# Performance work log

Measured on AMD Instinct MI355X. Metric: run time of the kernel, lower is better.

## Reference

```python
import jax, jax.numpy as jnp
import numpy as np

B, H, N, D = 2, 12, 2048, 64
M = int(D * np.log(D))          # 266 performer random features
E3 = 3 * D                      # performer value hidden size = head_dim*3
DH2 = 2 * D                     # predictor enc hidden = head_dim*2
T = 128                         # attention_predictor_length
CHUNK = 128                     # chunk size for causal linear attention scan
KERNEL_EPS = 1e-3               # performer generalized-kernel epsilon
D_EPS = 1e-6                    # denominator epsilon (added to k_cumsum)
LN_EPS = 1e-5


def setup_inputs() -> dict:
    key = jax.random.key(0)
    ks = jax.random.split(key, 10)
    return {
        "q": jax.random.normal(ks[0], (B, H, N, D), jnp.float32),
        "k": jax.random.normal(ks[1], (B, H, N, D), jnp.float32),
        "v3": jax.random.normal(ks[2], (B, H, N, E3), jnp.float32),
        "proj": jax.random.normal(ks[3], (M, D), jnp.float32),
        "enc_w": jax.random.normal(ks[4], (E3, DH2), jnp.float32) * 0.05,
        "enc_b": jnp.zeros((DH2,), jnp.float32),
        "ln_g": jnp.ones((DH2,), jnp.float32),
        "ln_b": jnp.zeros((DH2,), jnp.float32),
        "dec_w": jax.random.normal(ks[5], (DH2, T), jnp.float32) * 0.05,
        "dec_b": jnp.zeros((T,), jnp.float32),
    }


def _generalized_features(x, proj):
    # performer generalized attention kernel: relu((x / d^0.25) @ proj^T) + eps
    dn = 1.0 / (x.shape[-1] ** 0.25)
    xp = jnp.einsum("bhnd,md->bhnm", x * dn, proj)
    return jax.nn.relu(xp) + KERNEL_EPS


def _causal_linear_attention(qf, kf, v):
    # qf, kf: [B,H,N,M]; v: [B,H,N,E]. Chunked recurrent form of
    # out[n] = (qf[n] . cumsum(kf)[n])^-1 * qf[n] @ cumsum(kf[m] v[m]^T)[n]
    nE = v.shape[-1]
    nc = N // CHUNK
    qc = qf.reshape(B, H, nc, CHUNK, M).transpose(2, 0, 1, 3, 4)
    kc = kf.reshape(B, H, nc, CHUNK, M).transpose(2, 0, 1, 3, 4)
    vc = v.reshape(B, H, nc, CHUNK, nE).transpose(2, 0, 1, 3, 4)
    mask = jnp.tril(jnp.ones((CHUNK, CHUNK), qf.dtype))

    def step(carry, inp):
        ksum, S = carry                      # [B,H,M], [B,H,M,E]
        q_c, k_c, v_c = inp                  # [B,H,C,M], [B,H,C,M], [B,H,C,E]
        qk = jnp.einsum("bhim,bhjm->bhij", q_c, k_c) * mask  # causal within chunk
        # denominator: qf[n] . (k_cumsum[n] + eps)
        d = (jnp.einsum("bhcm,bhm->bhc", q_c, ksum)
             + qk.sum(-1)
             + D_EPS * q_c.sum(-1))
        out = (jnp.einsum("bhcm,bhme->bhce", q_c, S)
               + jnp.einsum("bhij,bhje->bhie", qk, v_c)) / d[..., None]
        ksum = ksum + k_c.sum(axis=2)
        S = S + jnp.einsum("bhcm,bhce->bhme", k_c, v_c)
        return (ksum, S), out

    init = (jnp.zeros((B, H, M), qf.dtype), jnp.zeros((B, H, M, nE), qf.dtype))
    _, outs = jax.lax.scan(step, init, (qc, kc, vc))
    return outs.transpose(1, 2, 0, 3, 4).reshape(B, H, N, nE)


def reference(q, k, v3, proj, enc_w, enc_b, ln_g, ln_b, dec_w, dec_b):
    qf = _generalized_features(q, proj)
    kf = _generalized_features(k, proj)
    ctx = _causal_linear_attention(qf, kf, v3)            # [B,H,N,3D]
    # attention predictor: Linear -> LayerNorm -> GELU -> Linear -> softmax
    h = jnp.einsum("bhne,ec->bhnc", ctx, enc_w) + enc_b    # [B,H,N,2D]
    mu = h.mean(-1, keepdims=True)
    var = ((h - mu) ** 2).mean(-1, keepdims=True)
    h = (h - mu) * jax.lax.rsqrt(var + LN_EPS) * ln_g + ln_b
    h = jax.nn.gelu(h, approximate=False)
    scores = jnp.einsum("bhnc,ct->bhnt", h, dec_w) + dec_b  # [B,H,N,T]
    est_probs = jax.nn.softmax(scores, axis=-1)
    return ctx, est_probs
```

## Files before the change

kernel.cpp:

```cpp
#include <hip/hip_runtime.h>
#include <hip/hip_bf16.h>
#include <math.h>

constexpr int Bn = 2, Hn = 12, BHn = 24;
constexpr int Nn = 2048, Dn = 64;
constexpr int Mn = 266, MPn = 272;
constexpr int E3n = 192, DHn = 128, Tn = 128;
constexpr int Cn = 128, NCn = 16;

#define DNRM 0.35355339059327373f
#define KEPS 1e-3f
#define DEPS 1e-6f
#define LNEPS 1e-5f

static const size_t OFF_QF   = 0;
static const size_t OFF_KF   = 26738688;
static const size_t OFF_QK   = 53477376;
static const size_t OFF_D    = 66060288;
static const size_t OFF_KPRE = 66256896;
static const size_t OFF_S    = 66674688;
static const size_t OFF_WT   = OFF_KF;
static const size_t WS_NEED  = 106782720;

using bf16x8 = __attribute__((ext_vector_type(8))) short;
using f32x4  = __attribute__((ext_vector_type(4))) float;

__device__ inline float u2f(unsigned int u) {
  union { float f; unsigned int i; } c; c.i = u << 16; return c.f;
}
__device__ inline unsigned short f2u(float x) {
  __hip_bfloat16 h = __float2bfloat16(x);
  unsigned short u; __builtin_memcpy(&u, &h, 2); return u;
}
__device__ inline void unpack8(uint4 v, float* a) {
  a[0] = u2f(v.x & 0xffffu); a[1] = u2f(v.x >> 16);
  a[2] = u2f(v.y & 0xffffu); a[3] = u2f(v.y >> 16);
  a[4] = u2f(v.z & 0xffffu); a[5] = u2f(v.z >> 16);
  a[6] = u2f(v.w & 0xffffu); a[7] = u2f(v.w >> 16);
}
__device__ inline ushort4 f4tobf(float4 v) {
  ushort4 o;
  o.x = f2u(v.x); o.y = f2u(v.y); o.z = f2u(v.z); o.w = f2u(v.w);
  return o;
}

__global__ __launch_bounds__(256) void k_features_mfma(
    const float* __restrict__ q, const float* __restrict__ k,
    const float* __restrict__ proj,
    unsigned short* __restrict__ qf, unsigned short* __restrict__ kf) {
  __shared__ unsigned short at[64][40];
  __shared__ unsigned short bt[272][40];
  const float* x = (blockIdx.y == 0) ? q : k;
  unsigned short* outp = (blockIdx.y == 0) ? qf : kf;
  int tid = threadIdx.x;
  int w = tid >> 6, l = tid & 63;
  int l16 = l & 15, lg = l >> 4;
  int r0 = blockIdx.x * 64;

  f32x4 acc[17] = {};
  for (int kt = 0; kt < 2; ++kt) {
    int k0 = kt * 32;
    __syncthreads();
    #pragma unroll
    for (int p = 0; p < 2; ++p) {
      int idx = tid + p * 256;
      int row = idx >> 3, kq = idx & 7;
      float4 v = *(const float4*)(x + (size_t)(r0 + row) * Dn + k0 + kq * 4);
      *(ushort4*)&at[row][kq * 4] = f4tobf(v);
    }
    for (int idx = tid; idx < 2176; idx += 256) {
      int mq = idx >> 3, kq = idx & 7;
      float4 v = make_float4(0.f, 0.f, 0.f, 0.f);
      if (mq < Mn) v = *(const float4*)(proj + (size_t)mq * Dn + k0 + kq * 4);
      *(ushort4*)&bt[mq][kq * 4] = f4tobf(v);
    }
    __syncthreads();
    bf16x8 a = *(const bf16x8*)((const char*)&at[0][0] + (w*16 + l16) * 80 + lg * 16);
    #pragma unroll
    for (int ct = 0; ct < 17; ++ct) {
      bf16x8 b = *(const bf16x8*)((const char*)&bt[0][0] + (ct*16 + l16) * 80 + lg * 16);
      acc[ct] = __builtin_amdgcn_mfma_f32_16x16x32_bf16(a, b, acc[ct], 0, 0, 0);
    }
  }
  #pragma unroll
  for (int ct = 0; ct < 17; ++ct)
    #pragma unroll
    for (int reg = 0; reg < 4; ++reg) {
      int row = r0 + w*16 + lg*4 + reg;
      int m = ct*16 + l16;
      float val = 0.f;
      if (m < Mn) val = fmaxf(acc[ct][reg] * DNRM, 0.f) + KEPS;
      outp[(size_t)row * MPn + m] = f2u(val);
    }
}

__global__ __launch_bounds__(256) void k_kprefix(float* __restrict__ kpre) {
  int bh = blockIdx.x; int tid = threadIdx.x;
  for (int m = tid; m < MPn; m += 256) {
    float v[NCn];
    #pragma unroll
    for (int c = 0; c < NCn; ++c) v[c] = kpre[((size_t)bh * NCn + c) * MPn + m];
    float acc = 0.f;
    #pragma unroll
    for (int c = 0; c < NCn; ++c) {
      kpre[((size_t)bh * NCn + c) * MPn + m] = acc;
      acc += v[c];
    }
  }
}

__global__ __launch_bounds__(256) void k_qk_mfma(
    const unsigned short* __restrict__ qf,
    const unsigned short* __restrict__ kf,
    const float* __restrict__ kpre,
    unsigned short* __restrict__ qkout,
    float* __restrict__ dden) {
  __shared__ unsigned short at[128][40];
  __shared__ unsigned short ktl[128][40];
  __shared__ float kp[MPn];
  __shared__ float rs_lds[128];
  int blk = blockIdx.x;
  int bh = blk >> 4, c = blk & 15;
  int tid = threadIdx.x;
  int w = tid >> 6, l = tid & 63;
  int l16 = l & 15, lg = l >> 4;
  size_t qbase = ((size_t)bh * Nn + (size_t)c * Cn) * MPn;
  size_t rbase = (size_t)bh * Nn + (size_t)c * Cn;
  for (int m = tid; m < MPn; m += 256) kp[m] = kpre[((size_t)bh * NCn + c) * MPn + m];

  f32x4 acc[2][8] = {};
  for (int kt = 0; kt < 9; ++kt) {
    int mt = kt * 32;
    __syncthreads();
    #pragma unroll
    for (int p = 0; p < 2; ++p) {
      int idx = tid * 8 + p * 2048;
      int r = idx >> 5, kk = idx & 31;
      uint4 va = make_uint4(0u,0u,0u,0u), vk = make_uint4(0u,0u,0u,0u);
      if (mt + kk < MPn) {
        va = *(const uint4*)(qf + qbase + (size_t)r * MPn + mt + kk);
        vk = *(const uint4*)(kf + qbase + (size_t)r * MPn + mt + kk);
      }
      *(uint4*)((char*)&at[0][0] + r * 80 + kk * 2) = va;
      *(uint4*)((char*)&ktl[0][0] + r * 80 + kk * 2) = vk;
    }
    __syncthreads();
    bf16x8 a0 = *(const bf16x8*)((const char*)&at[0][0] + (w*32 + l16) * 80 + lg * 16);
    bf16x8 a1 = *(const bf16x8*)((const char*)&at[0][0] + (w*32 + 16 + l16) * 80 + lg * 16);
    #pragma unroll
    for (int ct = 0; ct < 8; ++ct) {
      bf16x8 b = *(const bf16x8*)((const char*)&ktl[0][0] + (ct*16 + l16) * 80 + lg * 16);
      acc[0][ct] = __builtin_amdgcn_mfma_f32_16x16x32_bf16(a0, b, acc[0][ct], 0, 0, 0);
      acc[1][ct] = __builtin_amdgcn_mfma_f32_16x16x32_bf16(a1, b, acc[1][ct], 0, 0, 0);
    }
  }
  size_t qkbase = (size_t)blk * (Cn * Cn);
  float rs[2][4] = {};
  #pragma unroll
  for (int rt = 0; rt < 2; ++rt)
    #pragma unroll
    for (int ct = 0; ct < 8; ++ct)
      #pragma unroll
      for (int reg = 0; reg < 4; ++reg) {
        int row = w*32 + rt*16 + lg*4 + reg;
        int col = ct*16 + l16;
        float v = (col <= row) ? acc[rt][ct][reg] : 0.f;
        qkout[qkbase + (size_t)row * Cn + col] = f2u(v);
        rs[rt][reg] += v;
      }
  #pragma unroll
  for (int rt = 0; rt < 2; ++rt)
    #pragma unroll
    for (int reg = 0; reg < 4; ++reg) {
      float s = rs[rt][reg];
      s += __shfl_xor(s, 1); s += __shfl_xor(s, 2);
      s += __shfl_xor(s, 4); s += __shfl_xor(s, 8);
      rs[rt][reg] = s;
    }
  if (l16 == 0) {
    #pragma unroll
    for (int rt = 0; rt < 2; ++rt)
      #pragma unroll
      for (int reg = 0; reg < 4; ++reg)
        rs_lds[w*32 + rt*16 + lg*4 + reg] = rs[rt][reg];
  }
  __syncthreads();
  if (tid < 128) {
    float dot = 0.f, qs = 0.f;
    const unsigned short* qrow = qf + qbase + (size_t)tid * MPn;
    for (int m = 0; m < MPn; m += 8) {
      uint4 v = *(const uint4*)(qrow + m);
      float a[8]; unpack8(v, a);
      #pragma unroll
      for (int t = 0; t < 8; ++t) { dot += a[t] * kp[m + t]; qs += a[t]; }
    }
    dden[rbase + tid] = rs_lds[tid] + dot + DEPS * qs;
  }
}

__global__ __launch_bounds__(384) void k_schunk_mfma(
    const unsigned short* __restrict__ kf,
    const float* __restrict__ v3,
    unsigned short* __restrict__ ST,
    float* __restrict__ kpre) {
  __shared__ unsigned short at[96][40];
  __shared__ unsigned short bt[272][40];
  int blk = blockIdx.x, ey = blockIdx.y;
  int bh = blk >> 4, c = blk & 15;
  int e0 = ey * 96;
  int tid = threadIdx.x;
  int w = tid >> 6, l = tid & 63;
  int l16 = l & 15, lg = l >> 4;
  size_t vbase = ((size_t)bh * Nn + (size_t)c * Cn) * E3n + e0;
  size_t kbase = ((size_t)bh * Nn + (size_t)c * Cn) * MPn;

  f32x4 acc[17] = {};
  float ks = 0.f;
  for (int kt = 0; kt < 4; ++kt) {
    int jt = kt * 32;
    __syncthreads();
    #pragma unroll
    for (int p = 0; p < 8; ++p) {
      int idx = tid + p * 384;
      int e = idx % 96, j = idx / 96;
      at[e][j] = f2u(v3[vbase + (size_t)(jt + j) * E3n + e]);
    }
    for (int idx = tid; idx < 8704; idx += 384) {
      int m = idx % 272, j = idx / 272;
      bt[m][j] = kf[kbase + (size_t)(jt + j) * MPn + m];
    }
    __syncthreads();
    bf16x8 a = *(const bf16x8*)((const char*)&at[0][0] + (w*16 + l16) * 80 + lg * 16);
    #pragma unroll
    for (int ct = 0; ct < 17; ++ct) {
      bf16x8 b = *(const bf16x8*)((const char*)&bt[0][0] + (ct*16 + l16) * 80 + lg * 16);
      acc[ct] = __builtin_amdgcn_mfma_f32_16x16x32_bf16(a, b, acc[ct], 0, 0, 0);
    }
    if (ey == 0 && tid < MPn) {
      #pragma unroll
      for (int jq = 0; jq < 4; ++jq) {
        uint4 v = *(const uint4*)((const char*)&bt[0][0] + tid * 80 + jq * 16);
        float a8[8]; unpack8(v, a8);
        #pragma unroll
        for (int t = 0; t < 8; ++t) ks += a8[t];
      }
    }
  }
  size_t stbase = (size_t)blk * MPn * E3n + (size_t)e0 * MPn;
  #pragma unroll
  for (int ct = 0; ct < 17; ++ct)
    #pragma unroll
    for (int reg = 0; reg < 4; ++reg) {
      int e_loc = w*16 + lg*4 + reg;
      ST[stbase + (size_t)e_loc * MPn + ct*16 + l16] = f2u(acc[ct][reg]);
    }
  if (ey == 0 && tid < MPn)
    kpre[((size_t)bh * NCn + c) * MPn + tid] = ks;
}

__global__ __launch_bounds__(256) void k_wt(const float* __restrict__ enc_w,
    const float* __restrict__ dec_w, unsigned short* __restrict__ ewt,
    unsigned short* __restrict__ dwt) {
  int i = blockIdx.x * 256 + threadIdx.x;
  if (i < 128 * 192) {
    int n = i / 192, e = i - n * 192;
    ewt[i] = f2u(enc_w[(size_t)e * DHn + n]);
  } else {
    int j = i - 128 * 192;
    int t = j >> 7, c = j & 127;
    dwt[(size_t)t * DHn + c] = f2u(dec_w[(size_t)c * Tn + t]);
  }
}

__global__ __launch_bounds__(256) void k_sprefix(unsigned short* __restrict__ S) {
  int bh = blockIdx.x / 51, sub = blockIdx.x % 51;
  int idx4 = sub * 256 + threadIdx.x;
  size_t off = (size_t)idx4 * 4;
  ushort4 v[NCn];
  #pragma unroll
  for (int c = 0; c < NCn; ++c)
    v[c] = *(const ushort4*)(S + ((size_t)(bh * NCn + c)) * MPn * E3n + off);
  float a0 = 0.f, a1 = 0.f, a2 = 0.f, a3 = 0.f;
  #pragma unroll
  for (int c = 0; c < NCn; ++c) {
    ushort4 o;
    unsigned short* op = (unsigned short*)&o;
    op[0] = f2u(a0); op[1] = f2u(a1); op[2] = f2u(a2); op[3] = f2u(a3);
    *(ushort4*)(S + ((size_t)(bh * NCn + c)) * MPn * E3n + off) = o;
    a0 += u2f(v[c].x); a1 += u2f(v[c].y); a2 += u2f(v[c].z); a3 += u2f(v[c].w);
  }
}

__global__ __launch_bounds__(256) void k_ctx_mfma(
    const unsigned short* __restrict__ qf,
    const unsigned short* __restrict__ qkm,
    const unsigned short* __restrict__ ST,
    const float* __restrict__ v3,
    const float* __restrict__ dden,
    float* __restrict__ ctx) {
  __shared__ unsigned short at[128][40];
  __shared__ unsigned short bt[64][40];
  __shared__ float dd[128];
  int blk = blockIdx.x, ey = blockIdx.y;
  int bh = blk >> 4, c = blk & 15;
  int e0 = ey * 64;
  int tid = threadIdx.x;
  int w = tid >> 6, l = tid & 63;
  int l16 = l & 15, lg = l >> 4;
  size_t qbase = ((size_t)bh * Nn + (size_t)c * Cn) * MPn;
  size_t sbase = (size_t)blk * MPn * E3n + (size_t)e0 * MPn;
  size_t rbase = (size_t)bh * Nn + (size_t)c * Cn;
  if (tid < 128) dd[tid] = dden[rbase + tid];

  f32x4 acc[2][4] = {};
  for (int kt = 0; kt < 9; ++kt) {
    int mt = kt * 32;
    __syncthreads();
    #pragma unroll
    for (int p = 0; p < 2; ++p) {
      int idx = tid * 8 + p * 2048;
      int r = idx >> 5, kk = idx & 31;
      uint4 v = make_uint4(0u,0u,0u,0u);
      if (mt + kk < MPn) v = *(const uint4*)(qf + qbase + (size_t)r * MPn + mt + kk);
      *(uint4*)((char*)&at[0][0] + r * 80 + kk * 2) = v;
    }
    {
      int r = tid >> 2, kk = (tid & 3) * 8;
      uint4 v = make_uint4(0u,0u,0u,0u);
      if (mt + kk < MPn) v = *(const uint4*)(ST + sbase + (size_t)r * MPn + mt + kk);
      *(uint4*)((char*)&bt[0][0] + r * 80 + kk * 2) = v;
    }
    __syncthreads();
    bf16x8 a0 = *(const bf16x8*)((const char*)&at[0][0] + (w*32 + l16) * 80 + lg * 16);
    bf16x8 a1 = *(const bf16x8*)((const char*)&at[0][0] + (w*32 + 16 + l16) * 80 + lg * 16);
    #pragma unroll
    for (int ct = 0; ct < 4; ++ct) {
      bf16x8 b = *(const bf16x8*)((const char*)&bt[0][0] + (ct*16 + l16) * 80 + lg * 16);
      acc[0][ct] = __builtin_amdgcn_mfma_f32_16x16x32_bf16(a0, b, acc[0][ct], 0, 0, 0);
      acc[1][ct] = __builtin_amdgcn_mfma_f32_16x16x32_bf16(a1, b, acc[1][ct], 0, 0, 0);
    }
  }
  size_t kkbase = (size_t)blk * (Cn * Cn);
  size_t vb3 = ((size_t)bh * Nn + (size_t)c * Cn) * E3n + e0;
  for (int kt = 0; kt < 4; ++kt) {
    int jt = kt * 32;
    __syncthreads();
    #pragma unroll
    for (int p = 0; p < 2; ++p) {
      int idx = tid * 8 + p * 2048;
      int r = idx >> 5, kk = idx & 31;
      uint4 v = *(const uint4*)(qkm + kkbase + (size_t)r * Cn + jt + kk);
      *(uint4*)((char*)&at[0][0] + r * 80 + kk * 2) = v;
    }
    #pragma unroll
    for (int p = 0; p < 8; ++p) {
      int idx = tid + p * 256;
      int e = idx & 63, j = idx >> 6;
      bt[e][j] = f2u(v3[vb3 + (size_t)j * E3n + e]);
    }
    __syncthreads();
    bf16x8 a0 = *(const bf16x8*)((const char*)&at[0][0] + (w*32 + l16) * 80 + lg * 16);
    bf16x8 a1 = *(const bf16x8*)((const char*)&at[0][0] + (w*32 + 16 + l16) * 80 + lg * 16);
    #pragma unroll
    for (int ct = 0; ct < 4; ++ct) {
      bf16x8 b = *(const bf16x8*)((const char*)&bt[0][0] + (ct*16 + l16) * 80 + lg * 16);
      acc[0][ct] = __builtin_amdgcn_mfma_f32_16x16x32_bf16(a0, b, acc[0][ct], 0, 0, 0);
      acc[1][ct] = __builtin_amdgcn_mfma_f32_16x16x32_bf16(a1, b, acc[1][ct], 0, 0, 0);
    }
    vb3 += 32 * E3n;
  }
  #pragma unroll
  for (int rt = 0; rt < 2; ++rt)
    #pragma unroll
    for (int ct = 0; ct < 4; ++ct)
      #pragma unroll
      for (int reg = 0; reg < 4; ++reg) {
        int row = w*32 + rt*16 + lg*4 + reg;
        float inv = 1.f / dd[row];
        ctx[(rbase + row) * (size_t)E3n + e0 + ct*16 + l16] = acc[rt][ct][reg] * inv;
      }
}

__global__ __launch_bounds__(256) void k_pred_fused(
    const float* __restrict__ ctx,
    const unsigned short* __restrict__ ewt,
    const unsigned short* __restrict__ dwt,
    const float* __restrict__ enc_b, const float* __restrict__ ln_g,
    const float* __restrict__ ln_b, const float* __restrict__ dec_b,
    float* __restrict__ probs) {
  __shared__ unsigned short at[128][40];
  __shared__ unsigned short bt[128][40];
  __shared__ unsigned short ht[128][200];
  int tid = threadIdx.x;
  int w = tid >> 6, l = tid & 63;
  int l16 = l & 15, lg = l >> 4;
  size_t r0 = (size_t)blockIdx.x * 128;

  float ebv[8], ggv[8], llv[8], dbv[8];
  #pragma unroll
  for (int ct = 0; ct < 8; ++ct) {
    ebv[ct] = enc_b[ct*16 + l16];
    ggv[ct] = ln_g[ct*16 + l16];
    llv[ct] = ln_b[ct*16 + l16];
    dbv[ct] = dec_b[ct*16 + l16];
  }

  f32x4 acc1[2][8] = {};
  for (int kt = 0; kt < 6; ++kt) {
    int k0 = kt * 32;
    __syncthreads();
    #pragma unroll
    for (int p = 0; p < 4; ++p) {
      int idx = tid + p * 256;
      int row = idx >> 3, kq = idx & 7;
      float4 v = *(const float4*)(ctx + (r0 + row) * E3n + k0 + kq * 4);
      *(ushort4*)&at[row][kq * 4] = f4tobf(v);
    }
    #pragma unroll
    for (int p = 0; p < 2; ++p) {
      int idx = tid + p * 256;
      int n = idx >> 2, kq = idx & 3;
      *(uint4*)&bt[n][kq * 8] = *(const uint4*)(ewt + (size_t)n * E3n + k0 + kq * 8);
    }
    __syncthreads();
    bf16x8 a0 = *(const bf16x8*)((const char*)&at[0][0] + (w*32 + l16) * 80 + lg * 16);
    bf16x8 a1 = *(const bf16x8*)((const char*)&at[0][0] + (w*32 + 16 + l16) * 80 + lg * 16);
    #pragma unroll
    for (int ct = 0; ct < 8; ++ct) {
      bf16x8 b = *(const bf16x8*)((const char*)&bt[0][0] + (ct*16 + l16) * 80 + lg * 16);
      acc1[0][ct] = __builtin_amdgcn_mfma_f32_16x16x32_bf16(a0, b, acc1[0][ct], 0, 0, 0);
      acc1[1][ct] = __builtin_amdgcn_mfma_f32_16x16x32_bf16(a1, b, acc1[1][ct], 0, 0, 0);
    }
  }
  #pragma unroll
  for (int rt = 0; rt < 2; ++rt) {
    #pragma unroll
    for (int reg = 0; reg < 4; ++reg) {
      float hv[8];
      float s = 0.f, s2 = 0.f;
      #pragma unroll
      for (int ct = 0; ct < 8; ++ct) {
        float v = acc1[rt][ct][reg] + ebv[ct];
        hv[ct] = v; s += v; s2 += v * v;
      }
      #pragma unroll
      for (int m = 1; m < 16; m <<= 1) { s += __shfl_xor(s, m); s2 += __shfl_xor(s2, m); }
      float mu = s * (1.f / 128.f);
      float var = s2 * (1.f / 128.f) - mu * mu;
      float rsq = rsqrtf(var + LNEPS);
      int row = w*32 + rt*16 + lg*4 + reg;
      #pragma unroll
      for (int ct = 0; ct < 8; ++ct) {
        float v = (hv[ct] - mu) * rsq * ggv[ct] + llv[ct];
        v = 0.5f * v * (1.f + erff(v * 0.70710678118654752f));
        ht[row][ct*16 + l16] = f2u(v);
      }
    }
  }
  f32x4 acc2[2][8] = {};
  for (int kt = 0; kt < 4; ++kt) {
    int c0 = kt * 32;
    __syncthreads();
    #pragma unroll
    for (int p = 0; p < 2; ++p) {
      int idx = tid + p * 256;
      int t = idx >> 2, kq = idx & 3;
      *(uint4*)&bt[t][kq * 8] = *(const uint4*)(dwt + (size_t)t * DHn + c0 + kq * 8);
    }
    __syncthreads();
    bf16x8 a0 = *(const bf16x8*)&ht[w*32 + l16][c0 + lg*8];
    bf16x8 a1 = *(const bf16x8*)&ht[w*32 + 16 + l16][c0 + lg*8];
    #pragma unroll
    for (int ct = 0; ct < 8; ++ct) {
      bf16x8 b = *(const bf16x8*)((const char*)&bt[0][0] + (ct*16 + l16) * 80 + lg * 16);
      acc2[0][ct] = __builtin_amdgcn_mfma_f32_16x16x32_bf16(a0, b, acc2[0][ct], 0, 0, 0);
      acc2[1][ct] = __builtin_amdgcn_mfma_f32_16x16x32_bf16(a1, b, acc2[1][ct], 0, 0, 0);
    }
  }
  #pragma unroll
  for (int rt = 0; rt < 2; ++rt) {
    #pragma unroll
    for (int reg = 0; reg < 4; ++reg) {
      float sv[8];
      float m = -1e30f;
      #pragma unroll
      for (int ct = 0; ct < 8; ++ct) {
        sv[ct] = acc2[rt][ct][reg] + dbv[ct];
        m = fmaxf(m, sv[ct]);
      }
      #pragma unroll
      for (int mm = 1; mm < 16; mm <<= 1) m = fmaxf(m, __shfl_xor(m, mm));
      float s = 0.f;
      #pragma unroll
      for (int ct = 0; ct < 8; ++ct) { sv[ct] = expf(sv[ct] - m); s += sv[ct]; }
      #pragma unroll
      for (int mm = 1; mm < 16; mm <<= 1) s += __shfl_xor(s, mm);
      float inv = 1.f / s;
      int row = w*32 + rt*16 + lg*4 + reg;
      #pragma unroll
      for (int ct = 0; ct < 8; ++ct)
        probs[(r0 + row) * (size_t)Tn + ct*16 + l16] = sv[ct] * inv;
    }
  }
}

extern "C" void kernel_launch(void* const* d_in, const int* in_sizes, int n_in,
                              void* d_out, int out_size, void* d_ws, size_t ws_size,
                              hipStream_t stream) {
  const float* q     = (const float*)d_in[0];
  const float* k     = (const float*)d_in[1];
  const float* v3    = (const float*)d_in[2];
  const float* proj  = (const float*)d_in[3];
  const float* enc_w = (const float*)d_in[4];
  const float* enc_b = (const float*)d_in[5];
  const float* ln_g  = (const float*)d_in[6];
  const float* ln_b  = (const float*)d_in[7];
  const float* dec_w = (const float*)d_in[8];
  const float* dec_b = (const float*)d_in[9];
  float* out = (float*)d_out;
  char* ws = (char*)d_ws;
  if (ws_size < WS_NEED) return;

  unsigned short* qf   = (unsigned short*)(ws + OFF_QF);
  unsigned short* kf   = (unsigned short*)(ws + OFF_KF);
  unsigned short* qk   = (unsigned short*)(ws + OFF_QK);
  float*          dden = (float*)(ws + OFF_D);
  float*          kpre = (float*)(ws + OFF_KPRE);
  unsigned short* ST   = (unsigned short*)(ws + OFF_S);
  unsigned short* ewt  = (unsigned short*)(ws + OFF_WT);
  unsigned short* dwt  = (unsigned short*)(ws + OFF_WT + 49152);
  float* ctx   = out;
  float* probs = out + (size_t)BHn * Nn * E3n;

  k_features_mfma<<<dim3(BHn * Nn / 64, 2), 256, 0, stream>>>(q, k, proj, qf, kf);
  k_schunk_mfma <<<dim3(BHn * NCn, 2),  384, 0, stream>>>(kf, v3, ST, kpre);
  k_kprefix     <<<dim3(BHn),           256, 0, stream>>>(kpre);
  k_qk_mfma     <<<dim3(BHn * NCn),     256, 0, stream>>>(qf, kf, kpre, qk, dden);
  k_wt          <<<dim3(160),           256, 0, stream>>>(enc_w, dec_w, ewt, dwt);
  k_sprefix     <<<dim3(BHn * 51),      256, 0, stream>>>(ST);
  k_ctx_mfma    <<<dim3(BHn * NCn, 3),  256, 0, stream>>>(qf, qk, ST, v3, dden, ctx);
  k_pred_fused  <<<dim3(BHn * Nn / 128),256, 0, stream>>>(ctx, ewt, dwt, enc_b, ln_g,
                                                          ln_b, dec_b, probs);
}
```

Before: 182.4 us.

## Stage schunk loads through LDS with vector reads and use 64-wide e tiles

The S-chunk kernel now loads v3 and kf tiles with coalesced float4/uint4 global reads into staging LDS buffers, then transposes inside LDS instead of doing scattered scalar global loads. It also switches to 256-thread blocks with 64-wide e tiles over 3 grid columns, and changes the LDS row pitch to 34 elements. The ctx kernel uses a new 34-pitch transposed buffer for the v tile. The aim is cheaper global access and fewer LDS bank conflicts, at the cost of an extra LDS pass and barrier, and a 68-byte row stride that is not 16-byte aligned for the bf16x8 vector reads.

```diff
diff --git a/kernel.cpp b/kernel.cpp
--- a/kernel.cpp
+++ b/kernel.cpp
@@ -198,16 +198,18 @@
   }
 }
 
-__global__ __launch_bounds__(384) void k_schunk_mfma(
+__global__ __launch_bounds__(256) void k_schunk_mfma(
     const unsigned short* __restrict__ kf,
     const float* __restrict__ v3,
     unsigned short* __restrict__ ST,
     float* __restrict__ kpre) {
-  __shared__ unsigned short at[96][40];
-  __shared__ unsigned short bt[272][40];
+  __shared__ unsigned short at[64][34];
+  __shared__ unsigned short bt[272][34];
+  __shared__ float vtmp[32][68];
+  __shared__ unsigned short ktmp[32][280];
   int blk = blockIdx.x, ey = blockIdx.y;
   int bh = blk >> 4, c = blk & 15;
-  int e0 = ey * 96;
+  int e0 = ey * 64;
   int tid = threadIdx.x;
   int w = tid >> 6, l = tid & 63;
   int l16 = l & 15, lg = l >> 4;
@@ -215,34 +217,56 @@
   size_t kbase = ((size_t)bh * Nn + (size_t)c * Cn) * MPn;
 
   f32x4 acc[17] = {};
-  float ks = 0.f;
+  float ks0 = 0.f, ks1 = 0.f;
   for (int kt = 0; kt < 4; ++kt) {
     int jt = kt * 32;
     __syncthreads();
     #pragma unroll
+    for (int p = 0; p < 2; ++p) {
+      int idx = tid + p * 256;
+      int row = idx >> 4, c4 = idx & 15;
+      *(float4*)&vtmp[row][c4 * 4] =
+          *(const float4*)(v3 + vbase + (size_t)(jt + row) * E3n + c4 * 4);
+    }
+    for (int idx = tid; idx < 1088; idx += 256) {
+      int row = idx / 34, c8 = idx % 34;
+      *(uint4*)&ktmp[row][c8 * 8] =
+          *(const uint4*)(kf + kbase + (size_t)(jt + row) * MPn + c8 * 8);
+    }
+    __syncthreads();
+    #pragma unroll
     for (int p = 0; p < 8; ++p) {
-      int idx = tid + p * 384;
-      int e = idx % 96, j = idx / 96;
-      at[e][j] = f2u(v3[vbase + (size_t)(jt + j) * E3n + e]);
-    }
-    for (int idx = tid; idx < 8704; idx += 384) {
+      int idx = tid + p * 256;
+      int e = idx & 63, j = idx >> 6;
+      at[e][j] = f2u(vtmp[j][e]);
+    }
+    for (int idx = tid; idx < 8704; idx += 256) {
       int m = idx % 272, j = idx / 272;
-      bt[m][j] = kf[kbase + (size_t)(jt + j) * MPn + m];
-    }
-    __syncthreads();
-    bf16x8 a = *(const bf16x8*)((const char*)&at[0][0] + (w*16 + l16) * 80 + lg * 16);
+      bt[m][j] = ktmp[j][m];
+    }
+    __syncthreads();
+    bf16x8 a = *(const bf16x8*)((const char*)&at[0][0] + (w*16 + l16) * 68 + lg * 16);
     #pragma unroll
     for (int ct = 0; ct < 17; ++ct) {
-      bf16x8 b = *(const bf16x8*)((const char*)&bt[0][0] + (ct*16 + l16) * 80 + lg * 16);
+      bf16x8 b = *(const bf16x8*)((const char*)&bt[0][0] + (ct*16 + l16) * 68 + lg * 16);
       acc[ct] = __builtin_amdgcn_mfma_f32_16x16x32_bf16(a, b, acc[ct], 0, 0, 0);
     }
-    if (ey == 0 && tid < MPn) {
+    if (ey == 0) {
       #pragma unroll
       for (int jq = 0; jq < 4; ++jq) {
-        uint4 v = *(const uint4*)((const char*)&bt[0][0] + tid * 80 + jq * 16);
+        uint4 v = *(const uint4*)((const char*)&bt[0][0] + tid * 68 + jq * 16);
         float a8[8]; unpack8(v, a8);
         #pragma unroll
-        for (int t = 0; t < 8; ++t) ks += a8[t];
+        for (int t = 0; t < 8; ++t) ks0 += a8[t];
+      }
+      if (tid < 16) {
+        #pragma unroll
+        for (int jq = 0; jq < 4; ++jq) {
+          uint4 v = *(const uint4*)((const char*)&bt[0][0] + (tid + 256) * 68 + jq * 16);
+          float a8[8]; unpack8(v, a8);
+          #pragma unroll
+          for (int t = 0; t < 8; ++t) ks1 += a8[t];
+        }
       }
     }
   }
@@ -254,8 +278,11 @@
       int e_loc = w*16 + lg*4 + reg;
       ST[stbase + (size_t)e_loc * MPn + ct*16 + l16] = f2u(acc[ct][reg]);
     }
-  if (ey == 0 && tid < MPn)
-    kpre[((size_t)bh * NCn + c) * MPn + tid] = ks;
+  if (ey == 0) {
+    kpre[((size_t)bh * NCn + c) * MPn + tid] = ks0;
+    if (tid < 16)
+      kpre[((size_t)bh * NCn + c) * MPn + tid + 256] = ks1;
+  }
 }
 
 __global__ __launch_bounds__(256) void k_wt(const float* __restrict__ enc_w,
@@ -300,6 +327,7 @@
     float* __restrict__ ctx) {
   __shared__ unsigned short at[128][40];
   __shared__ unsigned short bt[64][40];
+  __shared__ unsigned short bt2[64][34];
   __shared__ float dd[128];
   int blk = blockIdx.x, ey = blockIdx.y;
   int bh = blk >> 4, c = blk & 15;
@@ -356,14 +384,14 @@
     for (int p = 0; p < 8; ++p) {
       int idx = tid + p * 256;
       int e = idx & 63, j = idx >> 6;
-      bt[e][j] = f2u(v3[vb3 + (size_t)j * E3n + e]);
+      bt2[e][j] = f2u(v3[vb3 + (size_t)j * E3n + e]);
     }
     __syncthreads();
     bf16x8 a0 = *(const bf16x8*)((const char*)&at[0][0] + (w*32 + l16) * 80 + lg * 16);
     bf16x8 a1 = *(const bf16x8*)((const char*)&at[0][0] + (w*32 + 16 + l16) * 80 + lg * 16);
     #pragma unroll
     for (int ct = 0; ct < 4; ++ct) {
-      bf16x8 b = *(const bf16x8*)((const char*)&bt[0][0] + (ct*16 + l16) * 80 + lg * 16);
+      bf16x8 b = *(const bf16x8*)((const char*)&bt2[0][0] + (ct*16 + l16) * 68 + lg * 16);
       acc[0][ct] = __builtin_amdgcn_mfma_f32_16x16x32_bf16(a0, b, acc[0][ct], 0, 0, 0);
       acc[1][ct] = __builtin_amdgcn_mfma_f32_16x16x32_bf16(a1, b, acc[1][ct], 0, 0, 0);
     }
@@ -533,7 +561,7 @@
   float* probs = out + (size_t)BHn * Nn * E3n;
 
   k_features_mfma<<<dim3(BHn * Nn / 64, 2), 256, 0, stream>>>(q, k, proj, qf, kf);
-  k_schunk_mfma <<<dim3(BHn * NCn, 2),  384, 0, stream>>>(kf, v3, ST, kpre);
+  k_schunk_mfma <<<dim3(BHn * NCn, 3),  256, 0, stream>>>(kf, v3, ST, kpre);
   k_kprefix     <<<dim3(BHn),           256, 0, stream>>>(kpre);
   k_qk_mfma     <<<dim3(BHn * NCn),     256, 0, stream>>>(qf, kf, kpre, qk, dden);
   k_wt          <<<dim3(160),           256, 0, stream>>>(enc_w, dec_w, ewt, dwt);
```

Measured after the change: 203.2 us. +11.4%, slower.
